# Kernel tuning notes

Measured on AMD Instinct MI355X. Metric: run time of the kernel, lower is better.

## Reference

```python
import jax, jax.numpy as jnp
import numpy as np

LOCAL_REGION = 16
GRANULARITY = 2048
INIT_RATIO = 8
EXPAND_RATIO = 2
C = 128
N_LAYERS = 5


def setup_inputs() -> dict:
    key = jax.random.key(0)
    ks = jax.random.split(key, 20)
    g = lambda k, s: jax.random.normal(k, s, dtype=jnp.float32) * 0.05
    z = lambda n: jnp.zeros((n,), jnp.float32)
    return {
        "batch_x": jax.random.normal(ks[0], (1, 16384, 4), dtype=jnp.float32),
        # PT: attr embedding (in_channel=1 -> 128), positional MLP (3->128->128)
        "attr_w": g(ks[1], (1, C)), "attr_b": z(C),
        "pos_w1": g(ks[2], (3, C)), "pos_b1": z(C),
        "pos_w2": g(ks[3], (C, C)), "pos_b2": z(C),
        # 5 self-attention layers over the K-neighborhood
        "wq": g(ks[4], (N_LAYERS, C, C)),
        "wk": g(ks[5], (N_LAYERS, C, C)),
        "wv": g(ks[6], (N_LAYERS, C, C)),
        "wout": g(ks[7], (C, C)), "bout": z(C),
        # mu/sigma head: 128 -> 64 -> 16 -> 2
        "ms_w1": g(ks[8], (C, 64)), "ms_b1": z(64),
        "ms_w2": g(ks[9], (64, 16)), "ms_b2": z(16),
        "ms_w3": g(ks[10], (16, 2)), "ms_b3": z(2),
    }


def _window_schedule(N):
    base = min(N // INIT_RATIO, GRANULARITY)
    win = base
    sched = []
    cursor = base
    while cursor < N:
        win = min(win * EXPAND_RATIO, GRANULARITY)
        sched.append((cursor, min(win, N - cursor)))
        cursor += win
    return sched


def _forward(batch_x, attr_w, attr_b, pos_w1, pos_b1, pos_w2, pos_b2,
             wq, wk, wv, wout, bout, ms_w1, ms_b1, ms_w2, ms_b2, ms_w3, ms_b3):
    B, N, _ = batch_x.shape
    total_bits = jnp.float32(0.0)
    for cur, w in _window_schedule(N):
        context = batch_x[:, :cur, :]
        target = batch_x[:, cur:cur + w, :]
        tg, ta = target[..., :3], target[..., 3:]    # [B,M,3], [B,M,1]
        cg, ca = context[..., :3], context[..., 3:]  # [B,Nc,3], [B,Nc,1]
        # knn_points: brute-force squared distances, K smallest
        d2 = (jnp.sum(tg * tg, -1)[:, :, None] + jnp.sum(cg * cg, -1)[:, None, :]
              - 2.0 * jnp.einsum('bmd,bnd->bmn', tg, cg))  # [B,M,Nc]
        _, idx = jax.lax.top_k(-d2, LOCAL_REGION)            # [B,M,K]
        # knn_gather
        gg = jnp.take_along_axis(cg[:, None], idx[..., None], axis=2)  # [B,M,K,3]
        ga = jnp.take_along_axis(ca[:, None], idx[..., None], axis=2)  # [B,M,K,1]
        # n_scale_ball: center each neighborhood, scale into unit ball
        gg = gg - jnp.mean(gg, axis=2, keepdims=True)
        r = jnp.max(jnp.linalg.norm(gg, axis=-1, keepdims=True), axis=2, keepdims=True)
        gg = gg / jnp.maximum(r, 1e-8)
        # PT: pos-encoded grouped self-attention, max-pool over K
        pos = jax.nn.relu(gg @ pos_w1 + pos_b1) @ pos_w2 + pos_b2  # [B,M,K,C]
        f = ga @ attr_w + attr_b + pos
        for l in range(N_LAYERS):
            q, k, v = f @ wq[l], f @ wk[l], f @ wv[l]
            a = jax.nn.softmax(jnp.einsum('bmkc,bmjc->bmkj', q, k)
                               / jnp.sqrt(jnp.float32(C)), axis=-1)
            f = f + jnp.einsum('bmkj,bmjc->bmkc', a, v)
        feat = jnp.max(f @ wout + bout, axis=2)  # [B,M,C]
        # mu/sigma head
        h = jax.nn.relu(feat @ ms_w1 + ms_b1)
        h = jax.nn.relu(h @ ms_w2 + ms_b2)
        ms = h @ ms_w3 + ms_b3
        mu, sigma = ms[..., :1], jnp.exp(ms[..., 1:])
        # feature_probs_based_mu_sigma: bits under quantized Gaussian
        inv = 1.0 / (sigma * jnp.sqrt(jnp.float32(2.0)))
        probs = 0.5 * (jax.lax.erf((ta + 0.5 - mu) * inv)
                       - jax.lax.erf((ta - 0.5 - mu) * inv))
        total_bits = total_bits + jnp.sum(jnp.clip(-jnp.log2(probs + 1e-10), 0.0, 50.0))
    return total_bits


def reference(batch_x, attr_w, attr_b, pos_w1, pos_b1, pos_w2, pos_b2,
              wq, wk, wv, wout, bout, ms_w1, ms_b1, ms_w2, ms_b2, ms_w3, ms_b3):
    return _forward(batch_x, attr_w, attr_b, pos_w1, pos_b1, pos_w2, pos_b2,
                    wq, wk, wv, wout, bout, ms_w1, ms_b1, ms_w2, ms_b2, ms_w3, ms_b3)
```

## Files before the change

### kernel.cpp

```cpp
#include <hip/hip_runtime.h>
#include <math.h>

#define NPTS 16384
#define WWIN 2048
#define NWIN 7
#define KNB  16
#define CDIM 128
#define NTGT (NPTS - WWIN)
#define TPB  4
#define NBLK (NTGT / TPB)
#define NMAT 12

typedef _Float16 f16;
typedef __attribute__((ext_vector_type(8))) _Float16 f16x8;
typedef __attribute__((ext_vector_type(4))) _Float16 f16x4;
typedef __attribute__((ext_vector_type(2))) _Float16 f16x2;
typedef __attribute__((ext_vector_type(4))) float f32x4;

#define MFMA16(a, b, c)  __builtin_amdgcn_mfma_f32_16x16x32_f16((a), (b), (c), 0, 0, 0)
#define MFMA16H(a, b, c) __builtin_amdgcn_mfma_f32_16x16x16f16((a), (b), (c), 0, 0, 0)

__device__ __forceinline__ unsigned umax_(unsigned a, unsigned b) { return a > b ? a : b; }
__device__ __forceinline__ unsigned umin_(unsigned a, unsigned b) { return a < b ? a : b; }

__global__ void prep_kernel(const float* __restrict__ pos_w2,
                            const float* __restrict__ wq,
                            const float* __restrict__ wk,
                            const float* __restrict__ wv,
                            const float* __restrict__ wout,
                            f16* __restrict__ wt) {
  const int i = blockIdx.x * 256 + threadIdx.x;
  if (i >= NMAT * 16384) return;
  const int mat = i >> 14;
  const int e   = i & 16383;
  const int k   = e >> 7;
  const int n   = e & 127;
  if (mat < 7) {
    const float* src = (mat == 0) ? pos_w2 : (mat <= 5 ? wv + (mat - 1) * 16384 : wout);
    wt[mat * 16384 + n * 128 + k] = (f16)src[k * 128 + n];
  } else {
    const int l = mat - 7;
    const float* qr = wq + l * 16384 + k * 128;
    const float* kr = wk + l * 16384 + n * 128;
    float sacc = 0.f;
#pragma unroll 4
    for (int c = 0; c < 128; ++c) sacc += qr[c] * kr[c];
    wt[mat * 16384 + n * 128 + k] = (f16)sacc;
  }
}

__device__ __forceinline__ f16x8 ldA(const f16* __restrict__ buf, int row0,
                                     int l15, int lg, int kc) {
  const int row = row0 + l15;
  const int col = (kc * 32 + lg * 8) ^ ((row & 7) << 3);
  return *(const f16x8*)(buf + row * 128 + col);
}

__device__ __forceinline__ void stD(f16* __restrict__ buf, int row0, int col0,
                                    int l15, int lg, const f32x4 v) {
#pragma unroll
  for (int r = 0; r < 4; ++r) {
    const int row = row0 + lg * 4 + r;
    const int col = (col0 + l15) ^ ((row & 7) << 3);
    buf[row * 128 + col] = (f16)v[r];
  }
}

__device__ __forceinline__ void zacc(f32x4 (&acc)[4][2]) {
#pragma unroll
  for (int mt = 0; mt < 4; ++mt)
#pragma unroll
    for (int nt = 0; nt < 2; ++nt) acc[mt][nt] = (f32x4){0.f, 0.f, 0.f, 0.f};
}

__device__ __forceinline__ void gemm_tile(const f16* __restrict__ src,
                                          const f16* __restrict__ wmat,
                                          int l15, int lg, int n0,
                                          f32x4 (&acc)[4][2]) {
#pragma unroll
  for (int kc = 0; kc < 4; ++kc) {
    const f16x8 b0 = *(const f16x8*)(wmat + (n0 + l15) * 128 + kc * 32 + lg * 8);
    const f16x8 b1 = *(const f16x8*)(wmat + (n0 + 16 + l15) * 128 + kc * 32 + lg * 8);
#pragma unroll
    for (int mt = 0; mt < 4; ++mt) {
      const f16x8 a = ldA(src, mt * 16, l15, lg, kc);
      acc[mt][0] = MFMA16(a, b0, acc[mt][0]);
      acc[mt][1] = MFMA16(a, b1, acc[mt][1]);
    }
  }
}

__global__ __launch_bounds__(256, 2)
void nn_kernel(
    const float4* __restrict__ bx, const f16* __restrict__ wt,
    const float* __restrict__ attr_w, const float* __restrict__ attr_b,
    const float* __restrict__ pos_w1, const float* __restrict__ pos_b1,
    const float* __restrict__ pos_b2, const float* __restrict__ bout,
    const float* __restrict__ ms_w1, const float* __restrict__ ms_b1,
    const float* __restrict__ ms_w2, const float* __restrict__ ms_b2,
    const float* __restrict__ ms_w3, const float* __restrict__ ms_b3,
    float* __restrict__ partials) {
  __shared__ __align__(16) f16 fA[64 * 128];
  __shared__ __align__(16) f16 qA[64 * 128];
  __shared__ __align__(16) char aux[4096];

  const int t     = threadIdx.x;
  const int wv    = t >> 6;
  const int lane  = t & 63;
  const int l15   = lane & 15;
  const int lg    = lane >> 4;
  const int n0    = wv * 32;
  const int slot0 = (NBLK - 1 - blockIdx.x) * TPB;

  f16* pAh = (f16*)aux;
  unsigned* nbr = (unsigned*)aux;
  float* ggs = (float*)(aux + 1024);

  {
    const int  slot = slot0 + wv;
    const int  cur  = WWIN * ((slot0 >> 11) + 1);
    const float4 tp = bx[WWIN + slot];

    unsigned u0 = 0xFFFFFFF0u, u1 = 0xFFFFFFF1u, u2 = 0xFFFFFFF2u, u3 = 0xFFFFFFF3u;

#define INS4(P) { const unsigned p_ = (P);                                     \
    const unsigned t0 = umax_(u0, p_); u0 = umin_(u0, p_);                     \
    const unsigned t1 = umax_(u1, t0); u1 = umin_(u1, t0);                     \
    const unsigned t2 = umax_(u2, t1); u2 = umin_(u2, t1);                     \
    u3 = umin_(u3, t2); }
#define PROC(CA, CB, JJ) {                                                     \
    const float dx0 = tp.x - (CA).x, dy0 = tp.y - (CA).y, dz0 = tp.z - (CA).z; \
    const float dx1 = tp.x - (CB).x, dy1 = tp.y - (CB).y, dz1 = tp.z - (CB).z; \
    const float d20 = dx0 * dx0 + dy0 * dy0 + dz0 * dz0;                       \
    const float d21 = dx1 * dx1 + dy1 * dy1 + dz1 * dz1;                       \
    const unsigned p0 = ((__float_as_uint(d20) << 1) & 0xFFFFC000u) | (unsigned)(JJ);      \
    const unsigned p1 = ((__float_as_uint(d21) << 1) & 0xFFFFC000u) | (unsigned)((JJ) + 64); \
    INS4(p0) INS4(p1) }

    float4 a0 = bx[lane],       b0 = bx[lane + 64];
    float4 a1 = bx[lane + 128], b1 = bx[lane + 192];
    float4 a2 = bx[lane + 256], b2 = bx[lane + 320];
    float4 a3 = bx[lane + 384], b3 = bx[lane + 448];
    for (int j = lane; j < cur; j += 512) {
      const float4 n0_ = bx[j + 512], n1_ = bx[j + 576];
      const float4 n2_ = bx[j + 640], n3_ = bx[j + 704];
      const float4 n4_ = bx[j + 768], n5_ = bx[j + 832];
      const float4 n6_ = bx[j + 896], n7_ = bx[j + 960];
      PROC(a0, b0, j)       a0 = n0_; b0 = n1_;
      PROC(a1, b1, j + 128) a1 = n2_; b1 = n3_;
      PROC(a2, b2, j + 256) a2 = n4_; b2 = n5_;
      PROC(a3, b3, j + 384) a3 = n6_; b3 = n7_;
    }
#undef PROC
#undef INS4

    for (int n = 0; n < 16; ++n) {
      unsigned m = u0;
      m = umin_(m, (unsigned)__shfl_xor((int)m, 1));
      m = umin_(m, (unsigned)__shfl_xor((int)m, 2));
      m = umin_(m, (unsigned)__shfl_xor((int)m, 4));
      m = umin_(m, (unsigned)__shfl_xor((int)m, 8));
      m = umin_(m, (unsigned)__shfl_xor((int)m, 16));
      m = umin_(m, (unsigned)__shfl_xor((int)m, 32));
      if (lane == n) nbr[wv * 16 + n] = m & 0x3FFFu;
      if (u0 == m) { u0 = u1; u1 = u2; u2 = u3; u3 = 0xFFFFFFFFu; }
    }
  }
  __syncthreads();

  if (t < 64) {
    const int nid  = (int)nbr[t];
    const float4 p = bx[nid];
    float sx = p.x, sy = p.y, sz = p.z;
#pragma unroll
    for (int m = 1; m < 16; m <<= 1) {
      sx += __shfl_xor(sx, m); sy += __shfl_xor(sy, m); sz += __shfl_xor(sz, m);
    }
    const float gx = p.x - sx * 0.0625f;
    const float gy = p.y - sy * 0.0625f;
    const float gz = p.z - sz * 0.0625f;
    float nr = sqrtf(gx * gx + gy * gy + gz * gz);
#pragma unroll
    for (int m = 1; m < 16; m <<= 1) nr = fmaxf(nr, __shfl_xor(nr, m));
    const float inv = 1.f / fmaxf(nr, 1e-8f);
    ggs[t * 4 + 0] = gx * inv; ggs[t * 4 + 1] = gy * inv;
    ggs[t * 4 + 2] = gz * inv; ggs[t * 4 + 3] = p.w;
  }
  __syncthreads();

  {
    const int row = t & 63;
    const int cb  = (t >> 6) * 32;
    const float gx = ggs[row * 4], gy = ggs[row * 4 + 1], gz = ggs[row * 4 + 2];
#pragma unroll
    for (int c = cb; c < cb + 32; c += 2) {
      const float h0 = pos_b1[c]     + gx * pos_w1[c]     + gy * pos_w1[128 + c]     + gz * pos_w1[256 + c];
      const float h1 = pos_b1[c + 1] + gx * pos_w1[c + 1] + gy * pos_w1[128 + c + 1] + gz * pos_w1[256 + c + 1];
      f16x2 pr; pr[0] = (f16)fmaxf(h0, 0.f); pr[1] = (f16)fmaxf(h1, 0.f);
      *(f16x2*)(qA + row * 128 + (c ^ ((row & 7) << 3))) = pr;
    }
  }
  __syncthreads();

  f32x4 facc[4][2];
  {
    zacc(facc);
    gemm_tile(qA, wt, l15, lg, n0, facc);
#pragma unroll
    for (int nt = 0; nt < 2; ++nt) {
      const int col = n0 + nt * 16 + l15;
      const float bias = pos_b2[col] + attr_b[col];
      const float aw   = attr_w[col];
#pragma unroll
      for (int mt = 0; mt < 4; ++mt) {
#pragma unroll
        for (int r = 0; r < 4; ++r)
          facc[mt][nt][r] += bias + ggs[(mt * 16 + lg * 4 + r) * 4 + 3] * aw;
        stD(fA, mt * 16, n0 + nt * 16, l15, lg, facc[mt][nt]);
      }
    }
  }
  __syncthreads();

  for (int l = 0; l < 5; ++l) {
    f16x4 vfrag[4][2];
    {
      f32x4 acc[4][2];
      zacc(acc);
      gemm_tile(fA, wt + (7 + l) * 16384, l15, lg, n0, acc);
#pragma unroll
      for (int mt = 0; mt < 4; ++mt)
#pragma unroll
        for (int nt = 0; nt < 2; ++nt)
          stD(qA, mt * 16, n0 + nt * 16, l15, lg, acc[mt][nt]);
      zacc(acc);
      gemm_tile(fA, wt + (1 + l) * 16384, l15, lg, n0, acc);
#pragma unroll
      for (int mt = 0; mt < 4; ++mt)
#pragma unroll
        for (int nt = 0; nt < 2; ++nt)
#pragma unroll
        for (int r = 0; r < 4; ++r)
          vfrag[mt][nt][r] = (f16)acc[mt][nt][r];
    }
    __syncthreads();
    {
      f32x4 s = (f32x4){0.f, 0.f, 0.f, 0.f};
#pragma unroll
      for (int kc = 0; kc < 4; ++kc)
        s = MFMA16(ldA(qA, wv * 16, l15, lg, kc), ldA(fA, wv * 16, l15, lg, kc), s);
#pragma unroll
      for (int r = 0; r < 4; ++r) {
        float v = s[r] * 0.08838834764831844055f;
        float mx = v;
#pragma unroll
        for (int m = 1; m < 16; m <<= 1) mx = fmaxf(mx, __shfl_xor(mx, m));
        const float e = __expf(v - mx);
        float sm = e;
#pragma unroll
        for (int m = 1; m < 16; m <<= 1) sm += __shfl_xor(sm, m);
        pAh[wv * 256 + (lg * 4 + r) * 16 + l15] = (f16)(e / sm);
      }
    }
    __syncthreads();
    {
#pragma unroll
      for (int tt = 0; tt < 4; ++tt) {
        const f16x4 aP = *(const f16x4*)(pAh + tt * 256 + l15 * 16 + lg * 4);
#pragma unroll
        for (int nt = 0; nt < 2; ++nt) {
          facc[tt][nt] = MFMA16H(aP, vfrag[tt][nt], facc[tt][nt]);
          stD(fA, tt * 16, n0 + nt * 16, l15, lg, facc[tt][nt]);
        }
      }
    }
    __syncthreads();
  }

  float* feats = (float*)aux;
  float* h1s   = feats + 512;
  float* h2s   = h1s + 256;
  float* btmp  = h2s + 64;
  {
    f32x4 acc[4][2];
    zacc(acc);
    gemm_tile(fA, wt + 6 * 16384, l15, lg, n0, acc);
#pragma unroll
    for (int nt = 0; nt < 2; ++nt) {
      const int col = n0 + nt * 16 + l15;
      const float bo = bout[col];
#pragma unroll
      for (int mt = 0; mt < 4; ++mt) {
        const f32x4 v = acc[mt][nt];
        float m = fmaxf(fmaxf(v[0], v[1]), fmaxf(v[2], v[3])) + bo;
        m = fmaxf(m, __shfl_xor(m, 16));
        m = fmaxf(m, __shfl_xor(m, 32));
        if (lg == 0) feats[mt * 128 + col] = m;
      }
    }
  }
  __syncthreads();
  {
    const int tt = t >> 6, h = t & 63;
    float a = ms_b1[h];
#pragma unroll 4
    for (int c = 0; c < 128; ++c) a += feats[tt * 128 + c] * ms_w1[c * 64 + h];
    h1s[tt * 64 + h] = fmaxf(a, 0.f);
  }
  __syncthreads();
  if (t < 64) {
    const int tt = t >> 4, h = t & 15;
    float a = ms_b2[h];
#pragma unroll 4
    for (int c = 0; c < 64; ++c) a += h1s[tt * 64 + c] * ms_w2[c * 16 + h];
    h2s[tt * 16 + h] = fmaxf(a, 0.f);
  }
  __syncthreads();
  if (t < TPB) {
    float mu = ms_b3[0], lgs = ms_b3[1];
#pragma unroll
    for (int c = 0; c < 16; ++c) {
      mu  += h2s[t * 16 + c] * ms_w3[2 * c];
      lgs += h2s[t * 16 + c] * ms_w3[2 * c + 1];
    }
    const float sigma = expf(lgs);
    const float inv   = 1.f / (sigma * 1.41421356237309504880f);
    const float ta    = ((const float*)bx)[(WWIN + slot0 + t) * 4 + 3];
    const float p = 0.5f * (erff((ta + 0.5f - mu) * inv) - erff((ta - 0.5f - mu) * inv));
    float bits = -log2f(p + 1e-10f);
    btmp[t] = fminf(fmaxf(bits, 0.f), 50.f);
  }
  __syncthreads();
  if (t == 0) partials[blockIdx.x] = btmp[0] + btmp[1] + btmp[2] + btmp[3];
}

__global__ void reduce_kernel(const float* __restrict__ partials, float* __restrict__ out) {
  float s = 0.f;
  for (int i = threadIdx.x; i < NBLK; i += 256) s += partials[i];
#pragma unroll
  for (int m = 1; m < 64; m <<= 1) s += __shfl_xor(s, m);
  __shared__ float wsum[4];
  if ((threadIdx.x & 63) == 0) wsum[threadIdx.x >> 6] = s;
  __syncthreads();
  if (threadIdx.x == 0) out[0] = wsum[0] + wsum[1] + wsum[2] + wsum[3];
}

extern "C" void kernel_launch(void* const* d_in, const int* in_sizes, int n_in,
                              void* d_out, int out_size, void* d_ws, size_t ws_size,
                              hipStream_t stream) {
  const float4* bx     = (const float4*)d_in[0];
  const float* attr_w  = (const float*)d_in[1];
  const float* attr_b  = (const float*)d_in[2];
  const float* pos_w1  = (const float*)d_in[3];
  const float* pos_b1  = (const float*)d_in[4];
  const float* pos_w2  = (const float*)d_in[5];
  const float* pos_b2  = (const float*)d_in[6];
  const float* wq      = (const float*)d_in[7];
  const float* wk      = (const float*)d_in[8];
  const float* wv      = (const float*)d_in[9];
  const float* wout    = (const float*)d_in[10];
  const float* bout    = (const float*)d_in[11];
  const float* ms_w1   = (const float*)d_in[12];
  const float* ms_b1   = (const float*)d_in[13];
  const float* ms_w2   = (const float*)d_in[14];
  const float* ms_b2   = (const float*)d_in[15];
  const float* ms_w3   = (const float*)d_in[16];
  const float* ms_b3   = (const float*)d_in[17];

  f16*   wt       = (f16*)((char*)d_ws);
  float* partials = (float*)((char*)d_ws + (1u << 19));

  prep_kernel<<<(NMAT * 16384 + 255) / 256, 256, 0, stream>>>(pos_w2, wq, wk, wv, wout, wt);
  nn_kernel<<<NBLK, 256, 0, stream>>>(bx, wt, attr_w, attr_b,
                                      pos_w1, pos_b1, pos_b2, bout,
                                      ms_w1, ms_b1, ms_w2, ms_b2, ms_w3, ms_b3,
                                      partials);
  reduce_kernel<<<1, 256, 0, stream>>>(partials, (float*)d_out);
}
```

Measured before the change: 361.8 us.

## Give each wave its own target point and drop block-wide barriers

The per-block work is remapped so that each wavefront processes one target point end to end: its 16 neighbours, all 128 channels and every layer. Before, the four waves split the channels of four targets and met at __syncthreads between every stage. Each wave now keeps private LDS buffers and runs the full-width GEMMs (8 N-blocks × 4 K-chunks) on its own 16 rows, which removes all block barriers. Partials are written per target and the reduce loop covers NTGT entries. The cost is that each wave loads all 128 weight columns from global memory/L2 rather than a 32-column slice, so weight traffic per wave goes up.

```diff
diff --git a/kernel.cpp b/kernel.cpp
--- a/kernel.cpp
+++ b/kernel.cpp
@@ -49,43 +49,34 @@
   }
 }
 
-__device__ __forceinline__ f16x8 ldA(const f16* __restrict__ buf, int row0,
-                                     int l15, int lg, int kc) {
-  const int row = row0 + l15;
-  const int col = (kc * 32 + lg * 8) ^ ((row & 7) << 3);
-  return *(const f16x8*)(buf + row * 128 + col);
-}
-
-__device__ __forceinline__ void stD(f16* __restrict__ buf, int row0, int col0,
-                                    int l15, int lg, const f32x4 v) {
+__device__ __forceinline__ f16x8 ldAw(const f16* __restrict__ buf, int l15, int lg,
+                                      int kc) {
+  const int col = (kc * 32 + lg * 8) ^ ((l15 & 7) << 3);
+  return *(const f16x8*)(buf + l15 * 128 + col);
+}
+
+__device__ __forceinline__ void stDw(f16* __restrict__ buf, int col0, int l15, int lg,
+                                     const f32x4 v) {
 #pragma unroll
   for (int r = 0; r < 4; ++r) {
-    const int row = row0 + lg * 4 + r;
+    const int row = lg * 4 + r;
     const int col = (col0 + l15) ^ ((row & 7) << 3);
     buf[row * 128 + col] = (f16)v[r];
   }
 }
 
-__device__ __forceinline__ void zacc(f32x4 (&acc)[4][2]) {
-#pragma unroll
-  for (int mt = 0; mt < 4; ++mt)
-#pragma unroll
-    for (int nt = 0; nt < 2; ++nt) acc[mt][nt] = (f32x4){0.f, 0.f, 0.f, 0.f};
-}
-
-__device__ __forceinline__ void gemm_tile(const f16* __restrict__ src,
-                                          const f16* __restrict__ wmat,
-                                          int l15, int lg, int n0,
-                                          f32x4 (&acc)[4][2]) {
+__device__ __forceinline__ void gemmw(const f16* __restrict__ src,
+                                      const f16* __restrict__ wmat,
+                                      int l15, int lg, f32x4 (&acc)[8]) {
+#pragma unroll
+  for (int nb = 0; nb < 8; ++nb) acc[nb] = (f32x4){0.f, 0.f, 0.f, 0.f};
 #pragma unroll
   for (int kc = 0; kc < 4; ++kc) {
-    const f16x8 b0 = *(const f16x8*)(wmat + (n0 + l15) * 128 + kc * 32 + lg * 8);
-    const f16x8 b1 = *(const f16x8*)(wmat + (n0 + 16 + l15) * 128 + kc * 32 + lg * 8);
-#pragma unroll
-    for (int mt = 0; mt < 4; ++mt) {
-      const f16x8 a = ldA(src, mt * 16, l15, lg, kc);
-      acc[mt][0] = MFMA16(a, b0, acc[mt][0]);
-      acc[mt][1] = MFMA16(a, b1, acc[mt][1]);
+    const f16x8 a = ldAw(src, l15, lg, kc);
+#pragma unroll
+    for (int nb = 0; nb < 8; ++nb) {
+      const f16x8 b = *(const f16x8*)(wmat + (nb * 16 + l15) * 128 + kc * 32 + lg * 8);
+      acc[nb] = MFMA16(a, b, acc[nb]);
     }
   }
 }
@@ -100,24 +91,26 @@
     const float* __restrict__ ms_w2, const float* __restrict__ ms_b2,
     const float* __restrict__ ms_w3, const float* __restrict__ ms_b3,
     float* __restrict__ partials) {
-  __shared__ __align__(16) f16 fA[64 * 128];
-  __shared__ __align__(16) f16 qA[64 * 128];
-  __shared__ __align__(16) char aux[4096];
-
-  const int t     = threadIdx.x;
-  const int wv    = t >> 6;
-  const int lane  = t & 63;
-  const int l15   = lane & 15;
-  const int lg    = lane >> 4;
-  const int n0    = wv * 32;
+  __shared__ __align__(16) f16 fP[TPB * 2048];
+  __shared__ __align__(16) f16 gP[TPB * 2048];
+  __shared__ __align__(16) char auxP[TPB * 1024];
+
+  const int t    = threadIdx.x;
+  const int wv   = t >> 6;
+  const int lane = t & 63;
+  const int l15  = lane & 15;
+  const int lg   = lane >> 4;
   const int slot0 = (NBLK - 1 - blockIdx.x) * TPB;
-
-  f16* pAh = (f16*)aux;
-  unsigned* nbr = (unsigned*)aux;
-  float* ggs = (float*)(aux + 1024);
-
-  {
-    const int  slot = slot0 + wv;
+  const int slot  = slot0 + wv;
+
+  f16*  fw  = fP + wv * 2048;
+  f16*  gw  = gP + wv * 2048;
+  char* au  = auxP + wv * 1024;
+  unsigned* nbr = (unsigned*)au;
+  float*    ggs = (float*)(au + 64);
+  f16*      Pt  = (f16*)(au + 512);
+
+  {
     const int  cur  = WWIN * ((slot0 >> 11) + 1);
     const float4 tp = bx[WWIN + slot];
 
@@ -162,14 +155,13 @@
       m = umin_(m, (unsigned)__shfl_xor((int)m, 8));
       m = umin_(m, (unsigned)__shfl_xor((int)m, 16));
       m = umin_(m, (unsigned)__shfl_xor((int)m, 32));
-      if (lane == n) nbr[wv * 16 + n] = m & 0x3FFFu;
+      if (lane == n) nbr[n] = m & 0x3FFFu;
       if (u0 == m) { u0 = u1; u1 = u2; u2 = u3; u3 = 0xFFFFFFFFu; }
     }
   }
-  __syncthreads();
-
-  if (t < 64) {
-    const int nid  = (int)nbr[t];
+
+  if (lane < 16) {
+    const int nid  = (int)nbr[lane];
     const float4 p = bx[nid];
     float sx = p.x, sy = p.y, sz = p.z;
 #pragma unroll
@@ -183,160 +175,120 @@
 #pragma unroll
     for (int m = 1; m < 16; m <<= 1) nr = fmaxf(nr, __shfl_xor(nr, m));
     const float inv = 1.f / fmaxf(nr, 1e-8f);
-    ggs[t * 4 + 0] = gx * inv; ggs[t * 4 + 1] = gy * inv;
-    ggs[t * 4 + 2] = gz * inv; ggs[t * 4 + 3] = p.w;
-  }
-  __syncthreads();
-
-  {
-    const int row = t & 63;
-    const int cb  = (t >> 6) * 32;
+    ggs[lane * 4 + 0] = gx * inv; ggs[lane * 4 + 1] = gy * inv;
+    ggs[lane * 4 + 2] = gz * inv; ggs[lane * 4 + 3] = p.w;
+  }
+
+  {
+    const int row = l15;
+    const int cb  = lg * 32;
     const float gx = ggs[row * 4], gy = ggs[row * 4 + 1], gz = ggs[row * 4 + 2];
 #pragma unroll
     for (int c = cb; c < cb + 32; c += 2) {
       const float h0 = pos_b1[c]     + gx * pos_w1[c]     + gy * pos_w1[128 + c]     + gz * pos_w1[256 + c];
       const float h1 = pos_b1[c + 1] + gx * pos_w1[c + 1] + gy * pos_w1[128 + c + 1] + gz * pos_w1[256 + c + 1];
       f16x2 pr; pr[0] = (f16)fmaxf(h0, 0.f); pr[1] = (f16)fmaxf(h1, 0.f);
-      *(f16x2*)(qA + row * 128 + (c ^ ((row & 7) << 3))) = pr;
-    }
-  }
-  __syncthreads();
-
-  f32x4 facc[4][2];
-  {
-    zacc(facc);
-    gemm_tile(qA, wt, l15, lg, n0, facc);
-#pragma unroll
-    for (int nt = 0; nt < 2; ++nt) {
-      const int col = n0 + nt * 16 + l15;
+      *(f16x2*)(gw + row * 128 + (c ^ ((row & 7) << 3))) = pr;
+    }
+  }
+
+  f32x4 facc[8];
+  {
+    f32x4 acc[8];
+    gemmw(gw, wt, l15, lg, acc);
+#pragma unroll
+    for (int nb = 0; nb < 8; ++nb) {
+      const int col = nb * 16 + l15;
       const float bias = pos_b2[col] + attr_b[col];
       const float aw   = attr_w[col];
 #pragma unroll
-      for (int mt = 0; mt < 4; ++mt) {
-#pragma unroll
-        for (int r = 0; r < 4; ++r)
-          facc[mt][nt][r] += bias + ggs[(mt * 16 + lg * 4 + r) * 4 + 3] * aw;
-        stD(fA, mt * 16, n0 + nt * 16, l15, lg, facc[mt][nt]);
-      }
-    }
-  }
-  __syncthreads();
+      for (int r = 0; r < 4; ++r)
+        acc[nb][r] += bias + ggs[(lg * 4 + r) * 4 + 3] * aw;
+      facc[nb] = acc[nb];
+      stDw(fw, nb * 16, l15, lg, facc[nb]);
+    }
+  }
 
   for (int l = 0; l < 5; ++l) {
-    f16x4 vfrag[4][2];
-    {
-      f32x4 acc[4][2];
-      zacc(acc);
-      gemm_tile(fA, wt + (7 + l) * 16384, l15, lg, n0, acc);
-#pragma unroll
-      for (int mt = 0; mt < 4; ++mt)
-#pragma unroll
-        for (int nt = 0; nt < 2; ++nt)
-          stD(qA, mt * 16, n0 + nt * 16, l15, lg, acc[mt][nt]);
-      zacc(acc);
-      gemm_tile(fA, wt + (1 + l) * 16384, l15, lg, n0, acc);
-#pragma unroll
-      for (int mt = 0; mt < 4; ++mt)
-#pragma unroll
-        for (int nt = 0; nt < 2; ++nt)
-#pragma unroll
-        for (int r = 0; r < 4; ++r)
-          vfrag[mt][nt][r] = (f16)acc[mt][nt][r];
-    }
-    __syncthreads();
-    {
-      f32x4 s = (f32x4){0.f, 0.f, 0.f, 0.f};
-#pragma unroll
-      for (int kc = 0; kc < 4; ++kc)
-        s = MFMA16(ldA(qA, wv * 16, l15, lg, kc), ldA(fA, wv * 16, l15, lg, kc), s);
-#pragma unroll
-      for (int r = 0; r < 4; ++r) {
-        float v = s[r] * 0.08838834764831844055f;
-        float mx = v;
-#pragma unroll
-        for (int m = 1; m < 16; m <<= 1) mx = fmaxf(mx, __shfl_xor(mx, m));
-        const float e = __expf(v - mx);
-        float sm = e;
-#pragma unroll
-        for (int m = 1; m < 16; m <<= 1) sm += __shfl_xor(sm, m);
-        pAh[wv * 256 + (lg * 4 + r) * 16 + l15] = (f16)(e / sm);
-      }
-    }
-    __syncthreads();
-    {
-#pragma unroll
-      for (int tt = 0; tt < 4; ++tt) {
-        const f16x4 aP = *(const f16x4*)(pAh + tt * 256 + l15 * 16 + lg * 4);
-#pragma unroll
-        for (int nt = 0; nt < 2; ++nt) {
-          facc[tt][nt] = MFMA16H(aP, vfrag[tt][nt], facc[tt][nt]);
-          stD(fA, tt * 16, n0 + nt * 16, l15, lg, facc[tt][nt]);
-        }
-      }
-    }
-    __syncthreads();
-  }
-
-  float* feats = (float*)aux;
-  float* h1s   = feats + 512;
-  float* h2s   = h1s + 256;
-  float* btmp  = h2s + 64;
-  {
-    f32x4 acc[4][2];
-    zacc(acc);
-    gemm_tile(fA, wt + 6 * 16384, l15, lg, n0, acc);
-#pragma unroll
-    for (int nt = 0; nt < 2; ++nt) {
-      const int col = n0 + nt * 16 + l15;
-      const float bo = bout[col];
-#pragma unroll
-      for (int mt = 0; mt < 4; ++mt) {
-        const f32x4 v = acc[mt][nt];
-        float m = fmaxf(fmaxf(v[0], v[1]), fmaxf(v[2], v[3])) + bo;
-        m = fmaxf(m, __shfl_xor(m, 16));
-        m = fmaxf(m, __shfl_xor(m, 32));
-        if (lg == 0) feats[mt * 128 + col] = m;
-      }
-    }
-  }
-  __syncthreads();
-  {
-    const int tt = t >> 6, h = t & 63;
-    float a = ms_b1[h];
+    f32x4 acc[8];
+    gemmw(fw, wt + (7 + l) * 16384, l15, lg, acc);
+#pragma unroll
+    for (int nb = 0; nb < 8; ++nb) stDw(gw, nb * 16, l15, lg, acc[nb]);
+    f32x4 s = (f32x4){0.f, 0.f, 0.f, 0.f};
+#pragma unroll
+    for (int kc = 0; kc < 4; ++kc)
+      s = MFMA16(ldAw(gw, l15, lg, kc), ldAw(fw, l15, lg, kc), s);
+#pragma unroll
+    for (int r = 0; r < 4; ++r) {
+      float v = s[r] * 0.08838834764831844055f;
+      float mx = v;
+#pragma unroll
+      for (int m = 1; m < 16; m <<= 1) mx = fmaxf(mx, __shfl_xor(mx, m));
+      const float e = __expf(v - mx);
+      float sm = e;
+#pragma unroll
+      for (int m = 1; m < 16; m <<= 1) sm += __shfl_xor(sm, m);
+      Pt[(lg * 4 + r) * 16 + l15] = (f16)(e / sm);
+    }
+    const f16x4 aP = *(const f16x4*)(Pt + l15 * 16 + lg * 4);
+    gemmw(fw, wt + (1 + l) * 16384, l15, lg, acc);
+#pragma unroll
+    for (int nb = 0; nb < 8; ++nb) {
+      f16x4 vf;
+#pragma unroll
+      for (int r = 0; r < 4; ++r) vf[r] = (f16)acc[nb][r];
+      facc[nb] = MFMA16H(aP, vf, facc[nb]);
+      stDw(fw, nb * 16, l15, lg, facc[nb]);
+    }
+  }
+
+  float* feat = (float*)au;
+  float* h1s  = (float*)(au + 512);
+  float* h2s  = (float*)(au + 768);
+  {
+    f32x4 acc[8];
+    gemmw(fw, wt + 6 * 16384, l15, lg, acc);
+#pragma unroll
+    for (int nb = 0; nb < 8; ++nb) {
+      const int col = nb * 16 + l15;
+      float m = fmaxf(fmaxf(acc[nb][0], acc[nb][1]), fmaxf(acc[nb][2], acc[nb][3]))
+                + bout[col];
+      m = fmaxf(m, __shfl_xor(m, 16));
+      m = fmaxf(m, __shfl_xor(m, 32));
+      if (lg == 0) feat[col] = m;
+    }
+  }
+  {
+    float a = ms_b1[lane];
 #pragma unroll 4
-    for (int c = 0; c < 128; ++c) a += feats[tt * 128 + c] * ms_w1[c * 64 + h];
-    h1s[tt * 64 + h] = fmaxf(a, 0.f);
-  }
-  __syncthreads();
-  if (t < 64) {
-    const int tt = t >> 4, h = t & 15;
-    float a = ms_b2[h];
+    for (int c = 0; c < 128; ++c) a += feat[c] * ms_w1[c * 64 + lane];
+    h1s[lane] = fmaxf(a, 0.f);
+  }
+  if (lane < 16) {
+    float a = ms_b2[lane];
 #pragma unroll 4
-    for (int c = 0; c < 64; ++c) a += h1s[tt * 64 + c] * ms_w2[c * 16 + h];
-    h2s[tt * 16 + h] = fmaxf(a, 0.f);
-  }
-  __syncthreads();
-  if (t < TPB) {
+    for (int c = 0; c < 64; ++c) a += h1s[c] * ms_w2[c * 16 + lane];
+    h2s[lane] = fmaxf(a, 0.f);
+  }
+  if (lane == 0) {
     float mu = ms_b3[0], lgs = ms_b3[1];
 #pragma unroll
     for (int c = 0; c < 16; ++c) {
-      mu  += h2s[t * 16 + c] * ms_w3[2 * c];
-      lgs += h2s[t * 16 + c] * ms_w3[2 * c + 1];
+      mu  += h2s[c] * ms_w3[2 * c];
+      lgs += h2s[c] * ms_w3[2 * c + 1];
     }
     const float sigma = expf(lgs);
     const float inv   = 1.f / (sigma * 1.41421356237309504880f);
-    const float ta    = ((const float*)bx)[(WWIN + slot0 + t) * 4 + 3];
+    const float ta    = ((const float*)bx)[(WWIN + slot) * 4 + 3];
     const float p = 0.5f * (erff((ta + 0.5f - mu) * inv) - erff((ta - 0.5f - mu) * inv));
     float bits = -log2f(p + 1e-10f);
-    btmp[t] = fminf(fmaxf(bits, 0.f), 50.f);
-  }
-  __syncthreads();
-  if (t == 0) partials[blockIdx.x] = btmp[0] + btmp[1] + btmp[2] + btmp[3];
+    partials[slot] = fminf(fmaxf(bits, 0.f), 50.f);
+  }
 }
 
 __global__ void reduce_kernel(const float* __restrict__ partials, float* __restrict__ out) {
   float s = 0.f;
-  for (int i = threadIdx.x; i < NBLK; i += 256) s += partials[i];
+  for (int i = threadIdx.x; i < NTGT; i += 256) s += partials[i];
 #pragma unroll
   for (int m = 1; m < 64; m <<= 1) s += __shfl_xor(s, m);
   __shared__ float wsum[4];
```

After: 763.0 us. 111% more time.

## Split GEMM tiles into column halves and raise occupancy to three blocks per CU

Applied to the files above, without the earlier changes.

Each 64x32 output GEMM is now computed as two sequential 16-column halves, so only four accumulators are live at a time instead of eight. This lowers register pressure, and launch bounds are raised from 2 to 3 blocks per CU to use the freed registers for more resident waves. In exchange, the A fragments are reloaded from LDS once per half, doubling LDS reads in the GEMMs, and the tighter register budget could force spills.

```diff
diff --git a/kernel.cpp b/kernel.cpp
--- a/kernel.cpp
+++ b/kernel.cpp
@@ -66,31 +66,22 @@
   }
 }
 
-__device__ __forceinline__ void zacc(f32x4 (&acc)[4][2]) {
-#pragma unroll
-  for (int mt = 0; mt < 4; ++mt)
-#pragma unroll
-    for (int nt = 0; nt < 2; ++nt) acc[mt][nt] = (f32x4){0.f, 0.f, 0.f, 0.f};
-}
-
-__device__ __forceinline__ void gemm_tile(const f16* __restrict__ src,
+__device__ __forceinline__ void gemm_half(const f16* __restrict__ src,
                                           const f16* __restrict__ wmat,
-                                          int l15, int lg, int n0,
-                                          f32x4 (&acc)[4][2]) {
+                                          int l15, int lg, int ncol,
+                                          f32x4 (&acc)[4]) {
 #pragma unroll
   for (int kc = 0; kc < 4; ++kc) {
-    const f16x8 b0 = *(const f16x8*)(wmat + (n0 + l15) * 128 + kc * 32 + lg * 8);
-    const f16x8 b1 = *(const f16x8*)(wmat + (n0 + 16 + l15) * 128 + kc * 32 + lg * 8);
+    const f16x8 b = *(const f16x8*)(wmat + (ncol + l15) * 128 + kc * 32 + lg * 8);
 #pragma unroll
     for (int mt = 0; mt < 4; ++mt) {
       const f16x8 a = ldA(src, mt * 16, l15, lg, kc);
-      acc[mt][0] = MFMA16(a, b0, acc[mt][0]);
-      acc[mt][1] = MFMA16(a, b1, acc[mt][1]);
-    }
-  }
-}
-
-__global__ __launch_bounds__(256, 2)
+      acc[mt] = MFMA16(a, b, acc[mt]);
+    }
+  }
+}
+
+__global__ __launch_bounds__(256, 3)
 void nn_kernel(
     const float4* __restrict__ bx, const f16* __restrict__ wt,
     const float* __restrict__ attr_w, const float* __restrict__ attr_b,
@@ -202,12 +193,13 @@
   }
   __syncthreads();
 
-  f32x4 facc[4][2];
-  {
-    zacc(facc);
-    gemm_tile(qA, wt, l15, lg, n0, facc);
+  f32x4 facc[2][4];
+  {
 #pragma unroll
     for (int nt = 0; nt < 2; ++nt) {
+#pragma unroll
+      for (int mt = 0; mt < 4; ++mt) facc[nt][mt] = (f32x4){0.f, 0.f, 0.f, 0.f};
+      gemm_half(qA, wt, l15, lg, n0 + nt * 16, facc[nt]);
       const int col = n0 + nt * 16 + l15;
       const float bias = pos_b2[col] + attr_b[col];
       const float aw   = attr_w[col];
@@ -215,33 +207,37 @@
       for (int mt = 0; mt < 4; ++mt) {
 #pragma unroll
         for (int r = 0; r < 4; ++r)
-          facc[mt][nt][r] += bias + ggs[(mt * 16 + lg * 4 + r) * 4 + 3] * aw;
-        stD(fA, mt * 16, n0 + nt * 16, l15, lg, facc[mt][nt]);
+          facc[nt][mt][r] += bias + ggs[(mt * 16 + lg * 4 + r) * 4 + 3] * aw;
+        stD(fA, mt * 16, n0 + nt * 16, l15, lg, facc[nt][mt]);
       }
     }
   }
   __syncthreads();
 
   for (int l = 0; l < 5; ++l) {
-    f16x4 vfrag[4][2];
+    f16x4 vfrag[2][4];
     {
-      f32x4 acc[4][2];
-      zacc(acc);
-      gemm_tile(fA, wt + (7 + l) * 16384, l15, lg, n0, acc);
-#pragma unroll
-      for (int mt = 0; mt < 4; ++mt)
-#pragma unroll
-        for (int nt = 0; nt < 2; ++nt)
-          stD(qA, mt * 16, n0 + nt * 16, l15, lg, acc[mt][nt]);
-      zacc(acc);
-      gemm_tile(fA, wt + (1 + l) * 16384, l15, lg, n0, acc);
-#pragma unroll
-      for (int mt = 0; mt < 4; ++mt)
-#pragma unroll
-        for (int nt = 0; nt < 2; ++nt)
-#pragma unroll
-        for (int r = 0; r < 4; ++r)
-          vfrag[mt][nt][r] = (f16)acc[mt][nt][r];
+#pragma unroll
+      for (int nt = 0; nt < 2; ++nt) {
+        f32x4 acc[4];
+#pragma unroll
+        for (int mt = 0; mt < 4; ++mt) acc[mt] = (f32x4){0.f, 0.f, 0.f, 0.f};
+        gemm_half(fA, wt + (7 + l) * 16384, l15, lg, n0 + nt * 16, acc);
+#pragma unroll
+        for (int mt = 0; mt < 4; ++mt)
+          stD(qA, mt * 16, n0 + nt * 16, l15, lg, acc[mt]);
+      }
+#pragma unroll
+      for (int nt = 0; nt < 2; ++nt) {
+        f32x4 acc[4];
+#pragma unroll
+        for (int mt = 0; mt < 4; ++mt) acc[mt] = (f32x4){0.f, 0.f, 0.f, 0.f};
+        gemm_half(fA, wt + (1 + l) * 16384, l15, lg, n0 + nt * 16, acc);
+#pragma unroll
+        for (int mt = 0; mt < 4; ++mt)
+#pragma unroll
+          for (int r = 0; r < 4; ++r) vfrag[nt][mt][r] = (f16)acc[mt][r];
+      }
     }
     __syncthreads();
     {
@@ -269,8 +265,8 @@
         const f16x4 aP = *(const f16x4*)(pAh + tt * 256 + l15 * 16 + lg * 4);
 #pragma unroll
         for (int nt = 0; nt < 2; ++nt) {
-          facc[tt][nt] = MFMA16H(aP, vfrag[tt][nt], facc[tt][nt]);
-          stD(fA, tt * 16, n0 + nt * 16, l15, lg, facc[tt][nt]);
+          facc[nt][tt] = MFMA16H(aP, vfrag[nt][tt], facc[nt][tt]);
+          stD(fA, tt * 16, n0 + nt * 16, l15, lg, facc[nt][tt]);
         }
       }
     }
@@ -282,16 +278,17 @@
   float* h2s   = h1s + 256;
   float* btmp  = h2s + 64;
   {
-    f32x4 acc[4][2];
-    zacc(acc);
-    gemm_tile(fA, wt + 6 * 16384, l15, lg, n0, acc);
 #pragma unroll
     for (int nt = 0; nt < 2; ++nt) {
+      f32x4 acc[4];
+#pragma unroll
+      for (int mt = 0; mt < 4; ++mt) acc[mt] = (f32x4){0.f, 0.f, 0.f, 0.f};
+      gemm_half(fA, wt + 6 * 16384, l15, lg, n0 + nt * 16, acc);
       const int col = n0 + nt * 16 + l15;
       const float bo = bout[col];
 #pragma unroll
       for (int mt = 0; mt < 4; ++mt) {
-        const f32x4 v = acc[mt][nt];
+        const f32x4 v = acc[mt];
         float m = fmaxf(fmaxf(v[0], v[1]), fmaxf(v[2], v[3])) + bo;
         m = fmaxf(m, __shfl_xor(m, 16));
         m = fmaxf(m, __shfl_xor(m, 32));
```

Result: slower. 497.6 us (+37.5%).
